# Kernel tuning notes

Measured on AMD Instinct MI355X. Metric: run time of the kernel, lower is better.

## Reference

```python
import jax, jax.numpy as jnp
import numpy as np

DIM = 1024
HEADS = 16
DK = DIM // HEADS
B, LQ, LKV = 2, 2048, 2048


def setup_inputs() -> dict:
    key = jax.random.key(0)
    ks = jax.random.split(key, 12)
    s = 1.0 / np.sqrt(DIM)
    return {
        "output": jax.random.normal(ks[0], (B, LQ, DIM), jnp.float32),
        "context": jax.random.normal(ks[1], (B, LKV, DIM), jnp.float32),
        # torch nn.Linear(dim, dim): store as [in, out] so y = x @ W + b
        "Wq": jax.random.normal(ks[2], (DIM, DIM), jnp.float32) * s,
        "bq": jax.random.normal(ks[3], (DIM,), jnp.float32) * s,
        "Wk": jax.random.normal(ks[4], (DIM, DIM), jnp.float32) * s,
        "bk": jax.random.normal(ks[5], (DIM,), jnp.float32) * s,
        "Wv": jax.random.normal(ks[6], (DIM, DIM), jnp.float32) * s,
        "bv": jax.random.normal(ks[7], (DIM,), jnp.float32) * s,
        # linear_out: in = 2*dim, out = dim
        "Wo": jax.random.normal(ks[8], (2 * DIM, DIM), jnp.float32) * (1.0 / np.sqrt(2 * DIM)),
        "bo": jax.random.normal(ks[9], (DIM,), jnp.float32) * (1.0 / np.sqrt(2 * DIM)),
    }


def _to_batches(x):
    # [B, L, dim] -> [B*H, L, dk], same layout as the torch reshape/permute
    b, l, _ = x.shape
    return x.reshape(b, l, HEADS, DK).transpose(0, 2, 1, 3).reshape(b * HEADS, l, DK)


def reference(output, context, Wq, bq, Wk, bk, Wv, bv, Wo, bo):
    b, lq, dim = output.shape
    q = _to_batches(output @ Wq + bq)     # [B*H, Lq, dk]
    k = _to_batches(context @ Wk + bk)    # [B*H, Lkv, dk]
    v = _to_batches(context @ Wv + bv)    # [B*H, Lkv, dk]

    scores = jnp.einsum('bqd,bkd->bqk', q, k) / jnp.sqrt(jnp.asarray(DK, q.dtype))
    attn = jax.nn.softmax(scores, axis=-1)            # [B*H, Lq, Lkv]; dropout = identity at eval
    ctx = jnp.einsum('bqk,bkd->bqd', attn, v)          # [B*H, Lq, dk]

    # Faithful to the original (non-standard) reshape:
    # scores.transpose(1,2).contiguous().view(B, -1, dim)
    concat = ctx.transpose(0, 2, 1).reshape(b, -1, dim)  # [B, Lq, dim] (permuted layout)
    combined = jnp.concatenate([concat, output], axis=2)  # [B, Lq, 2*dim]
    out = jnp.tanh(combined @ Wo + bo)                     # [B, Lq, dim]
    return (out, attn)
```

## Files before the change

### kernel.cpp

```cpp
#include <hip/hip_runtime.h>
#include <math.h>
#include <stdint.h>

#define DIM_ 1024
#define HEADS_ 16
#define DK_ 64
#define B_ 2
#define L_ 2048
#define BH_ (B_*HEADS_)
#define M_ (B_*L_)

typedef __attribute__((ext_vector_type(4))) float f32x4;
typedef __attribute__((ext_vector_type(8))) short bf16x8;
typedef __attribute__((ext_vector_type(4))) short bf16x4;

#define QSCALE 0.18033688f

static __device__ __forceinline__ short f2bf(float f) {
    uint32_t u = __builtin_bit_cast(uint32_t, f);
    u += 0x7fffu + ((u >> 16) & 1u);
    return (short)(u >> 16);
}
static __device__ __forceinline__ void gload16(const void* g, void* l) {
    __builtin_amdgcn_global_load_lds(
        (const __attribute__((address_space(1))) unsigned int*)g,
        (__attribute__((address_space(3))) unsigned int*)l, 16, 0, 0);
}

__global__ __launch_bounds__(256)
void prep(const float* __restrict__ xout, const float* __restrict__ xctx,
          const float* __restrict__ Wq, const float* __restrict__ Wk,
          const float* __restrict__ Wv, const float* __restrict__ Wo,
          short* __restrict__ xoutb, short* __restrict__ xctxb,
          short* __restrict__ WqT, short* __restrict__ WkT,
          short* __restrict__ WvT, short* __restrict__ WoT)
{
    __shared__ float ts[64][65];
    const int bid = blockIdx.x;
    const int tid = threadIdx.x;
    if (bid < 4096) {
        const int id = bid * 256 + tid;
        const int nA = (M_ * DIM_) / 8;
        const float* src = (id < nA) ? xout : xctx;
        short* dst = (id < nA) ? xoutb : xctxb;
        const int c = (id < nA) ? id : id - nA;
        const f32x4 v0 = *(const f32x4*)&src[(size_t)c * 8];
        const f32x4 v1 = *(const f32x4*)&src[(size_t)c * 8 + 4];
        bf16x8 o;
#pragma unroll
        for (int i = 0; i < 4; ++i) { o[i] = f2bf(v0[i]); o[4 + i] = f2bf(v1[i]); }
        *(bf16x8*)&dst[(size_t)c * 8] = o;
        return;
    }
    const int flat = bid - 4096;
    const int z = flat >> 9;
    const int rem = flat & 511;
    const int K = (z == 3) ? 2 * DIM_ : DIM_;
    const int k0 = (rem & 31) * 64;
    if (k0 >= K) return;
    const int n0 = (rem >> 5) * 64;
    const float* W = (z == 0) ? Wq : (z == 1) ? Wk : (z == 2) ? Wv : Wo;
    short* WT = (z == 0) ? WqT : (z == 1) ? WkT : (z == 2) ? WvT : WoT;
    {
        const int k = tid >> 2, noff = (tid & 3) * 16;
#pragma unroll
        for (int i = 0; i < 4; ++i)
            *(f32x4*)&ts[k][noff + i * 4] =
                *(const f32x4*)&W[(size_t)(k0 + k) * DIM_ + n0 + noff + i * 4];
    }
    __syncthreads();
    {
        const int n = tid >> 2, koff = (tid & 3) * 16;
#pragma unroll
        for (int c = 0; c < 2; ++c) {
            bf16x8 o;
#pragma unroll
            for (int i = 0; i < 8; ++i) o[i] = f2bf(ts[koff + c * 8 + i][n]);
            *(bf16x8*)&WT[(size_t)(n0 + n) * K + k0 + koff + c * 8] = o;
        }
    }
}

__global__ __launch_bounds__(256)
void qkv_mfma(const short* __restrict__ xoutb, const short* __restrict__ xctxb,
              const short* __restrict__ WqT, const short* __restrict__ WkT,
              const short* __restrict__ WvT,
              const float* __restrict__ bq, const float* __restrict__ bk,
              const float* __restrict__ bv,
              short* __restrict__ qh, short* __restrict__ kh, short* __restrict__ vT)
{
    const int z = blockIdx.z;
    const short* A  = (z == 0) ? xoutb : xctxb;
    const short* Bt = (z == 0) ? WqT : (z == 1) ? WkT : WvT;
    const float* bias = (z == 0) ? bq : (z == 1) ? bk : bv;

    const int flat = blockIdx.y * 8 + blockIdx.x;
    const int wgs = (flat & 7) * 32 + (flat >> 3);
    const int col0 = (wgs & 7) * 128;
    const int row0 = (wgs >> 3) * 128;
    const int tid = threadIdx.x;
    const int lane = tid & 63;
    const int w = tid >> 6;
    const int wm = (w >> 1) * 64, wn = (w & 1) * 64;
    const int l15 = lane & 15, g = lane >> 4;
    const int sub = lane >> 3, slt = lane & 7;

    __shared__ short As[128 * 64];
    __shared__ short Bs[128 * 64];

    const short* pA[4]; const short* pB[4]; short* ldsA[4]; short* ldsB[4];
#pragma unroll
    for (int i = 0; i < 4; ++i) {
        const int r = w * 32 + i * 8 + sub;
        const int sc = ((slt ^ (r & 7)) * 8);
        pA[i] = A  + (size_t)(row0 + r) * DIM_ + sc;
        pB[i] = Bt + (size_t)(col0 + r) * DIM_ + sc;
        ldsA[i] = &As[(w * 32 + i * 8) * 64];
        ldsB[i] = &Bs[(w * 32 + i * 8) * 64];
    }

    f32x4 acc[4][4];
#pragma unroll
    for (int mi = 0; mi < 4; ++mi)
#pragma unroll
        for (int ni = 0; ni < 4; ++ni) acc[mi][ni] = (f32x4)0.f;

    for (int k0 = 0; k0 < DIM_; k0 += 64) {
#pragma unroll
        for (int i = 0; i < 4; ++i) {
            gload16(pA[i] + k0, ldsA[i]);
            gload16(pB[i] + k0, ldsB[i]);
        }
        __syncthreads();
        bf16x8 af[4][2], bfr[4][2];
#pragma unroll
        for (int mi = 0; mi < 4; ++mi) {
            const int wa = wm + mi * 16 + l15;
#pragma unroll
            for (int ks = 0; ks < 2; ++ks)
                af[mi][ks] = *(const bf16x8*)&As[wa * 64 + (((ks * 4 + g) ^ (wa & 7)) * 8)];
        }
#pragma unroll
        for (int ni = 0; ni < 4; ++ni) {
            const int wb = wn + ni * 16 + l15;
#pragma unroll
            for (int ks = 0; ks < 2; ++ks)
                bfr[ni][ks] = *(const bf16x8*)&Bs[wb * 64 + (((ks * 4 + g) ^ (wb & 7)) * 8)];
        }
        __builtin_amdgcn_s_setprio(1);
#pragma unroll
        for (int mi = 0; mi < 4; ++mi)
#pragma unroll
            for (int ni = 0; ni < 4; ++ni)
#pragma unroll
                for (int ks = 0; ks < 2; ++ks)
                    acc[mi][ni] = __builtin_amdgcn_mfma_f32_16x16x32_bf16(af[mi][ks], bfr[ni][ks], acc[mi][ni], 0, 0, 0);
        __builtin_amdgcn_s_setprio(0);
        __syncthreads();
    }

#pragma unroll
    for (int ni = 0; ni < 4; ++ni) {
        const int col = col0 + wn + ni * 16 + l15;
        const int h = col >> 6, dk = col & 63;
        const float bb = bias[col];
#pragma unroll
        for (int mi = 0; mi < 4; ++mi) {
            const int rowb = row0 + wm + mi * 16 + g * 4;
            const int b = rowb >> 11;
            const int l = rowb & (L_ - 1);
            const int bh = b * 16 + h;
            if (z == 2) {
                bf16x4 o;
#pragma unroll
                for (int r = 0; r < 4; ++r) o[r] = f2bf(acc[mi][ni][r] + bb);
                *(bf16x4*)&vT[(size_t)(bh * 64 + dk) * L_ + l] = o;
            } else {
                short* dst = (z == 0) ? qh : kh;
                const float sc = (z == 0) ? QSCALE : 1.0f;
#pragma unroll
                for (int r = 0; r < 4; ++r)
                    dst[((size_t)bh * L_ + l + r) * DK_ + dk] = f2bf((acc[mi][ni][r] + bb) * sc);
            }
        }
    }
}

__global__ __launch_bounds__(512, 8)
void attn_mfma(const short* __restrict__ qh, const short* __restrict__ kh,
               const short* __restrict__ vT,
               float* __restrict__ attn, short* __restrict__ ctxTb)
{
    const int bid = blockIdx.x;
    const int wg = (bid & 7) * 128 + (bid >> 3);
    const int bh = wg >> 5;
    const int q0 = (wg & 31) * 64;

    const int tid = threadIdx.x;
    const int lane = tid & 63;
    const int w = tid >> 6;
    const int wq = w >> 1, wk = w & 1;
    const int l15 = lane & 15, g = lane >> 4;

    __shared__ short SM[17408];
    short* const Kb0 = SM;
    short* const Kb1 = SM + 4096;
    short* const Vb  = SM + 8192;
    short* const Psb = SM + 12288;
    float* const stat = (float*)(SM + 16896);

    const short* kbase = kh + (size_t)bh * (L_ * DK_);
    const short* vbase = vT + (size_t)bh * (DK_ * L_);

    const int lr = lane >> 3, ls = lane & 7;
    const int srow = w * 8 + lr;
    const short* kSrc = kbase + (size_t)srow * DK_ + ((ls ^ (srow & 7)) * 8);
    const short* vSrc = vbase + (size_t)srow * L_ + ((ls ^ (srow & 7)) * 8);

    bf16x8 qf[2];
#pragma unroll
    for (int ks = 0; ks < 2; ++ks)
        qf[ks] = *(const bf16x8*)&qh[((size_t)bh * L_ + q0 + wq * 16 + l15) * DK_ + ks * 32 + g * 8];

    int kbOff[2][2], vbOff[4];
#pragma unroll
    for (int cc = 0; cc < 2; ++cc)
#pragma unroll
        for (int ks = 0; ks < 2; ++ks) {
            const int row = wk * 32 + cc * 16 + l15;
            kbOff[cc][ks] = row * 64 + (((ks * 4 + g) ^ (row & 7)) * 8);
        }
#pragma unroll
    for (int nf = 0; nf < 4; ++nf) {
        const int row = nf * 16 + l15;
        vbOff[nf] = row * 64 + (((wk * 4 + g) ^ (row & 7)) * 8);
    }

    float m[4], s[4];
#pragma unroll
    for (int r = 0; r < 4; ++r) { m[r] = -1e30f; s[r] = 0.f; }

#pragma unroll
    for (int i = 0; i < 3; ++i)
        gload16(kSrc + (size_t)i * 64 * DK_, SM + (i << 12) + w * 512);
    asm volatile("s_waitcnt vmcnt(2)" ::: "memory");
    __builtin_amdgcn_sched_barrier(0);
    __builtin_amdgcn_s_barrier();

    for (int t = 0; t < 32; ++t) {
        if (t < 29)
            gload16(kSrc + (size_t)(t + 3) * 64 * DK_, SM + (((t + 3) & 3) << 12) + w * 512);
        const short* kb = SM + ((t & 3) << 12);
        f32x4 sa[2];
#pragma unroll
        for (int cc = 0; cc < 2; ++cc) sa[cc] = (f32x4)0.f;
        __builtin_amdgcn_s_setprio(1);
#pragma unroll
        for (int cc = 0; cc < 2; ++cc)
#pragma unroll
            for (int ks = 0; ks < 2; ++ks)
                sa[cc] = __builtin_amdgcn_mfma_f32_16x16x32_bf16(qf[ks], *(const bf16x8*)&kb[kbOff[cc][ks]], sa[cc], 0, 0, 0);
        __builtin_amdgcn_s_setprio(0);
#pragma unroll
        for (int r = 0; r < 4; ++r) {
            const float tm = fmaxf(sa[0][r], sa[1][r]);
            const float mn = fmaxf(m[r], tm);
            s[r] = s[r] * exp2f(m[r] - mn) + exp2f(sa[0][r] - mn) + exp2f(sa[1][r] - mn);
            m[r] = mn;
        }
        if (t < 29)       { asm volatile("s_waitcnt vmcnt(2)" ::: "memory"); }
        else if (t == 29) { asm volatile("s_waitcnt vmcnt(1)" ::: "memory"); }
        else if (t == 30) { asm volatile("s_waitcnt vmcnt(0)" ::: "memory"); }
        __builtin_amdgcn_sched_barrier(0);
        if (t < 31) __builtin_amdgcn_s_barrier();
    }
#pragma unroll
    for (int mask = 1; mask <= 8; mask <<= 1) {
#pragma unroll
        for (int r = 0; r < 4; ++r) {
            const float mo = __shfl_xor(m[r], mask);
            const float so = __shfl_xor(s[r], mask);
            const float mn = fmaxf(m[r], mo);
            s[r] = s[r] * exp2f(m[r] - mn) + so * exp2f(mo - mn);
            m[r] = mn;
        }
    }
    if (l15 == 0) {
#pragma unroll
        for (int r = 0; r < 4; ++r) {
            stat[((wq * 2 + wk) * 16 + g * 4 + r) * 2 + 0] = m[r];
            stat[((wq * 2 + wk) * 16 + g * 4 + r) * 2 + 1] = s[r];
        }
    }
    gload16(kSrc, SM + w * 512);
    asm volatile("s_waitcnt lgkmcnt(0)" ::: "memory");
    __builtin_amdgcn_s_barrier();
    float inv_s[4];
#pragma unroll
    for (int r = 0; r < 4; ++r) {
        const float m0 = stat[((wq * 2 + 0) * 16 + g * 4 + r) * 2 + 0];
        const float s0 = stat[((wq * 2 + 0) * 16 + g * 4 + r) * 2 + 1];
        const float m1 = stat[((wq * 2 + 1) * 16 + g * 4 + r) * 2 + 0];
        const float s1 = stat[((wq * 2 + 1) * 16 + g * 4 + r) * 2 + 1];
        const float mn = fmaxf(m0, m1);
        m[r] = mn;
        inv_s[r] = 1.0f / (s0 * exp2f(m0 - mn) + s1 * exp2f(m1 - mn));
    }

    f32x4 cacc[4];
#pragma unroll
    for (int nf = 0; nf < 4; ++nf) cacc[nf] = (f32x4)0.f;

    float* attnB = attn + ((size_t)bh * L_ + q0) * L_;

    asm volatile("s_waitcnt vmcnt(0)" ::: "memory");
    __builtin_amdgcn_sched_barrier(0);
    __builtin_amdgcn_s_barrier();

    for (int t = 0; t < 32; ++t) {
        if (t) {
            asm volatile("s_waitcnt vmcnt(8)" ::: "memory");
            __builtin_amdgcn_sched_barrier(0);
            __builtin_amdgcn_s_barrier();
        }
        gload16(vSrc + t * 64, Vb + w * 512);
        {
            const int tn = (t < 31) ? t + 1 : t;
            gload16(kSrc + (size_t)tn * 64 * DK_, ((t & 1) ? Kb0 : Kb1) + w * 512);
        }
        const short* kb = (t & 1) ? Kb1 : Kb0;
        f32x4 sa[2];
#pragma unroll
        for (int cc = 0; cc < 2; ++cc) sa[cc] = (f32x4)0.f;
        __builtin_amdgcn_s_setprio(1);
#pragma unroll
        for (int cc = 0; cc < 2; ++cc)
#pragma unroll
            for (int ks = 0; ks < 2; ++ks)
                sa[cc] = __builtin_amdgcn_mfma_f32_16x16x32_bf16(qf[ks], *(const bf16x8*)&kb[kbOff[cc][ks]], sa[cc], 0, 0, 0);
        __builtin_amdgcn_s_setprio(0);
#pragma unroll
        for (int cc = 0; cc < 2; ++cc)
#pragma unroll
            for (int r = 0; r < 4; ++r) {
                const float p = exp2f(sa[cc][r] - m[r]) * inv_s[r];
                Psb[(wq * 16 + g * 4 + r) * 72 + wk * 32 + cc * 16 + l15] = f2bf(p);
                __builtin_nontemporal_store(
                    p, attnB + (size_t)(wq * 16 + g * 4 + r) * L_ + t * 64 + wk * 32 + cc * 16 + l15);
            }
        asm volatile("s_waitcnt vmcnt(9) lgkmcnt(0)" ::: "memory");
        __builtin_amdgcn_sched_barrier(0);
        __builtin_amdgcn_s_barrier();
        const bf16x8 pa = *(const bf16x8*)&Psb[(wq * 16 + l15) * 72 + wk * 32 + g * 8];
        __builtin_amdgcn_s_setprio(1);
#pragma unroll
        for (int nf = 0; nf < 4; ++nf)
            cacc[nf] = __builtin_amdgcn_mfma_f32_16x16x32_bf16(pa, *(const bf16x8*)&Vb[vbOff[nf]], cacc[nf], 0, 0, 0);
        __builtin_amdgcn_s_setprio(0);
    }

    __syncthreads();
    float* scr = (float*)Kb0;
    float* scr1 = (float*)Kb1;
    if (wk) {
#pragma unroll
        for (int nf = 0; nf < 4; ++nf) {
            float* p = (nf < 2) ? scr : scr1;
            *(f32x4*)&p[(((wq * 2) + (nf & 1)) * 64 + lane) * 4] = cacc[nf];
        }
    }
    __syncthreads();
    if (!wk) {
#pragma unroll
        for (int nf = 0; nf < 4; ++nf) {
            const float* p = (nf < 2) ? scr : scr1;
            const f32x4 o = cacc[nf] + *(const f32x4*)&p[(((wq * 2) + (nf & 1)) * 64 + lane) * 4];
            bf16x4 ob;
#pragma unroll
            for (int r = 0; r < 4; ++r) ob[r] = f2bf(o[r]);
            *(bf16x4*)&ctxTb[(size_t)(bh * 64 + nf * 16 + l15) * L_ + q0 + wq * 16 + g * 4] = ob;
        }
    }
}

__global__ __launch_bounds__(256)
void out_mfma(const short* __restrict__ ctxTb, const short* __restrict__ xoutb,
              const short* __restrict__ WoT, const float* __restrict__ bo,
              float* __restrict__ out)
{
    const int flat = blockIdx.y * 16 + blockIdx.x;
    const int wgs = (flat & 7) * 64 + (flat >> 3);
    const int col0 = (wgs & 15) * 64;
    const int row0 = (wgs >> 4) * 128;
    const int tid = threadIdx.x;
    const int lane = tid & 63;
    const int w = tid >> 6;
    const int wm = (w >> 1) * 64, wn = (w & 1) * 32;
    const int l15 = lane & 15, g = lane >> 4;
    const int sub = lane >> 3, slt = lane & 7;

    __shared__ short As[128 * 64];
    __shared__ short Bs[64 * 64];

    const short* pA1[4]; const short* pA2[4]; const short* pB[2];
    short* ldsA[4]; short* ldsB[2];
#pragma unroll
    for (int i = 0; i < 4; ++i) {
        const int r = w * 32 + i * 8 + sub;
        const int rr = row0 + r;
        const int b = rr >> 11, l_ = rr & (L_ - 1);
        const int bh = b * 16 + (l_ >> 7), d = (l_ & 127) >> 1;
        const size_t off1 = ((size_t)(bh * 64 + d) << 11) + (size_t)((l_ & 1) << 10);
        const int sc = ((slt ^ (r & 7)) * 8);
        pA1[i] = ctxTb + off1 + sc;
        pA2[i] = xoutb + (size_t)rr * DIM_ + sc;
        ldsA[i] = &As[(w * 32 + i * 8) * 64];
    }
#pragma unroll
    for (int i = 0; i < 2; ++i) {
        const int r = w * 16 + i * 8 + sub;
        const int sc = ((slt ^ (r & 7)) * 8);
        pB[i]  = WoT + (size_t)(col0 + r) * (2 * DIM_) + sc;
        ldsB[i] = &Bs[(w * 16 + i * 8) * 64];
    }

    f32x4 acc[4][2];
#pragma unroll
    for (int mi = 0; mi < 4; ++mi)
#pragma unroll
        for (int ni = 0; ni < 2; ++ni) acc[mi][ni] = (f32x4)0.f;

    for (int k0 = 0; k0 < 2 * DIM_; k0 += 64) {
        const bool first = (k0 < DIM_);
        const int kk = first ? k0 : k0 - DIM_;
#pragma unroll
        for (int i = 0; i < 4; ++i)
            gload16(first ? (pA1[i] + kk) : (pA2[i] + kk), ldsA[i]);
#pragma unroll
        for (int i = 0; i < 2; ++i)
            gload16(pB[i] + k0, ldsB[i]);
        __syncthreads();
        bf16x8 af[4][2], bfr[2][2];
#pragma unroll
        for (int mi = 0; mi < 4; ++mi) {
            const int wa = wm + mi * 16 + l15;
#pragma unroll
            for (int ks = 0; ks < 2; ++ks)
                af[mi][ks] = *(const bf16x8*)&As[wa * 64 + (((ks * 4 + g) ^ (wa & 7)) * 8)];
        }
#pragma unroll
        for (int ni = 0; ni < 2; ++ni) {
            const int wb = wn + ni * 16 + l15;
#pragma unroll
            for (int ks = 0; ks < 2; ++ks)
                bfr[ni][ks] = *(const bf16x8*)&Bs[wb * 64 + (((ks * 4 + g) ^ (wb & 7)) * 8)];
        }
        __builtin_amdgcn_s_setprio(1);
#pragma unroll
        for (int mi = 0; mi < 4; ++mi)
#pragma unroll
            for (int ni = 0; ni < 2; ++ni)
#pragma unroll
                for (int ks = 0; ks < 2; ++ks)
                    acc[mi][ni] = __builtin_amdgcn_mfma_f32_16x16x32_bf16(af[mi][ks], bfr[ni][ks], acc[mi][ni], 0, 0, 0);
        __builtin_amdgcn_s_setprio(0);
        __syncthreads();
    }

#pragma unroll
    for (int ni = 0; ni < 2; ++ni) {
        const int col = col0 + wn + ni * 16 + l15;
        const float bb = bo[col];
#pragma unroll
        for (int mi = 0; mi < 4; ++mi) {
            const int rowb = row0 + wm + mi * 16 + g * 4;
#pragma unroll
            for (int r = 0; r < 4; ++r)
                out[(size_t)(rowb + r) * DIM_ + col] = tanhf(acc[mi][ni][r] + bb);
        }
    }
}

extern "C" void kernel_launch(void* const* d_in, const int* in_sizes, int n_in,
                              void* d_out, int out_size, void* d_ws, size_t ws_size,
                              hipStream_t stream)
{
    const float* xout = (const float*)d_in[0];
    const float* xctx = (const float*)d_in[1];
    const float* Wq = (const float*)d_in[2];
    const float* bq = (const float*)d_in[3];
    const float* Wk = (const float*)d_in[4];
    const float* bk = (const float*)d_in[5];
    const float* Wv = (const float*)d_in[6];
    const float* bv = (const float*)d_in[7];
    const float* Wo = (const float*)d_in[8];
    const float* bo = (const float*)d_in[9];

    float* out  = (float*)d_out;
    float* attn = out + (size_t)M_ * DIM_;

    short* ws = (short*)d_ws;
    short* xoutb = ws;
    short* xctxb = xoutb + (size_t)M_ * DIM_;
    short* WqT   = xctxb + (size_t)M_ * DIM_;
    short* WkT   = WqT + (size_t)DIM_ * DIM_;
    short* WvT   = WkT + (size_t)DIM_ * DIM_;
    short* WoT   = WvT + (size_t)DIM_ * DIM_;
    short* qh    = WoT + (size_t)2 * DIM_ * DIM_;
    short* kh    = qh + (size_t)BH_ * L_ * DK_;
    short* vT    = kh + (size_t)BH_ * L_ * DK_;
    short* ctxTb = vT + (size_t)BH_ * L_ * DK_;

    prep<<<6144, 256, 0, stream>>>(xout, xctx, Wq, Wk, Wv, Wo,
                                   xoutb, xctxb, WqT, WkT, WvT, WoT);
    qkv_mfma<<<dim3(8, 32, 3), 256, 0, stream>>>(
        xoutb, xctxb, WqT, WkT, WvT, bq, bk, bv, qh, kh, vT);
    attn_mfma<<<1024, 512, 0, stream>>>(qh, kh, vT, attn, ctxTb);
    out_mfma<<<dim3(16, 32), 256, 0, stream>>>(ctxTb, xoutb, WoT, bo, out);
}
```

Before: 279.2 us.

## Double-buffer LDS tiles in QKV projection and output GEMM kernels

Both the QKV projection GEMM and the output-projection GEMM now use two LDS buffers. The next K-tile's global-to-LDS load is issued before computing on the current tile, and each step ends with a single explicit waitcnt plus barrier. The aim is to hide global load latency behind MFMA work instead of stalling on every tile. In exchange the kernels use twice the shared memory, which may cut occupancy, and correctness now relies on manual vmcnt and barrier ordering.

```diff
diff --git a/kernel.cpp b/kernel.cpp
--- a/kernel.cpp
+++ b/kernel.cpp
@@ -105,18 +105,17 @@
     const int l15 = lane & 15, g = lane >> 4;
     const int sub = lane >> 3, slt = lane & 7;
 
-    __shared__ short As[128 * 64];
-    __shared__ short Bs[128 * 64];
-
-    const short* pA[4]; const short* pB[4]; short* ldsA[4]; short* ldsB[4];
+    __shared__ short As[2 * 128 * 64];
+    __shared__ short Bs[2 * 128 * 64];
+
+    const short* pA[4]; const short* pB[4]; int ldsOff[4];
 #pragma unroll
     for (int i = 0; i < 4; ++i) {
         const int r = w * 32 + i * 8 + sub;
         const int sc = ((slt ^ (r & 7)) * 8);
         pA[i] = A  + (size_t)(row0 + r) * DIM_ + sc;
         pB[i] = Bt + (size_t)(col0 + r) * DIM_ + sc;
-        ldsA[i] = &As[(w * 32 + i * 8) * 64];
-        ldsB[i] = &Bs[(w * 32 + i * 8) * 64];
+        ldsOff[i] = (w * 32 + i * 8) * 64;
     }
 
     f32x4 acc[4][4];
@@ -125,39 +124,68 @@
 #pragma unroll
         for (int ni = 0; ni < 4; ++ni) acc[mi][ni] = (f32x4)0.f;
 
-    for (int k0 = 0; k0 < DIM_; k0 += 64) {
-#pragma unroll
-        for (int i = 0; i < 4; ++i) {
-            gload16(pA[i] + k0, ldsA[i]);
-            gload16(pB[i] + k0, ldsB[i]);
-        }
-        __syncthreads();
-        bf16x8 af[4][2], bfr[4][2];
-#pragma unroll
-        for (int mi = 0; mi < 4; ++mi) {
-            const int wa = wm + mi * 16 + l15;
-#pragma unroll
-            for (int ks = 0; ks < 2; ++ks)
-                af[mi][ks] = *(const bf16x8*)&As[wa * 64 + (((ks * 4 + g) ^ (wa & 7)) * 8)];
-        }
-#pragma unroll
-        for (int ni = 0; ni < 4; ++ni) {
-            const int wb = wn + ni * 16 + l15;
-#pragma unroll
-            for (int ks = 0; ks < 2; ++ks)
-                bfr[ni][ks] = *(const bf16x8*)&Bs[wb * 64 + (((ks * 4 + g) ^ (wb & 7)) * 8)];
-        }
-        __builtin_amdgcn_s_setprio(1);
-#pragma unroll
-        for (int mi = 0; mi < 4; ++mi)
-#pragma unroll
-            for (int ni = 0; ni < 4; ++ni)
-#pragma unroll
-                for (int ks = 0; ks < 2; ++ks)
-                    acc[mi][ni] = __builtin_amdgcn_mfma_f32_16x16x32_bf16(af[mi][ks], bfr[ni][ks], acc[mi][ni], 0, 0, 0);
-        __builtin_amdgcn_s_setprio(0);
-        __syncthreads();
-    }
+#define QKV_STAGE(koff, buf)                                        \
+    {                                                               \
+        _Pragma("unroll")                                           \
+        for (int i = 0; i < 4; ++i) {                               \
+            gload16(pA[i] + (koff), As + (buf) * 8192 + ldsOff[i]); \
+            gload16(pB[i] + (koff), Bs + (buf) * 8192 + ldsOff[i]); \
+        }                                                           \
+    }
+
+#define QKV_COMPUTE(buf)                                                              \
+    {                                                                                 \
+        const short* as = As + (buf) * 8192;                                          \
+        const short* bs = Bs + (buf) * 8192;                                          \
+        bf16x8 af[4][2], bfr[4][2];                                                   \
+        _Pragma("unroll")                                                             \
+        for (int mi = 0; mi < 4; ++mi) {                                              \
+            const int wa = wm + mi * 16 + l15;                                        \
+            _Pragma("unroll")                                                         \
+            for (int ks = 0; ks < 2; ++ks)                                            \
+                af[mi][ks] = *(const bf16x8*)&as[wa * 64 + (((ks * 4 + g) ^ (wa & 7)) * 8)]; \
+        }                                                                             \
+        _Pragma("unroll")                                                             \
+        for (int ni = 0; ni < 4; ++ni) {                                              \
+            const int wb = wn + ni * 16 + l15;                                        \
+            _Pragma("unroll")                                                         \
+            for (int ks = 0; ks < 2; ++ks)                                            \
+                bfr[ni][ks] = *(const bf16x8*)&bs[wb * 64 + (((ks * 4 + g) ^ (wb & 7)) * 8)]; \
+        }                                                                             \
+        __builtin_amdgcn_s_setprio(1);                                                \
+        _Pragma("unroll")                                                             \
+        for (int mi = 0; mi < 4; ++mi)                                                \
+            _Pragma("unroll")                                                         \
+            for (int ni = 0; ni < 4; ++ni)                                            \
+                _Pragma("unroll")                                                     \
+                for (int ks = 0; ks < 2; ++ks)                                        \
+                    acc[mi][ni] = __builtin_amdgcn_mfma_f32_16x16x32_bf16(af[mi][ks], bfr[ni][ks], acc[mi][ni], 0, 0, 0); \
+        __builtin_amdgcn_s_setprio(0);                                                \
+    }
+
+    QKV_STAGE(0, 0);
+    asm volatile("s_waitcnt vmcnt(0)" ::: "memory");
+    __builtin_amdgcn_sched_barrier(0);
+    __builtin_amdgcn_s_barrier();
+
+    for (int kp = 0; kp < DIM_; kp += 128) {
+        QKV_STAGE(kp + 64, 1);
+        QKV_COMPUTE(0);
+        asm volatile("s_waitcnt vmcnt(0)" ::: "memory");
+        __builtin_amdgcn_sched_barrier(0);
+        __builtin_amdgcn_s_barrier();
+        if (kp + 128 < DIM_) {
+            QKV_STAGE(kp + 128, 0);
+            QKV_COMPUTE(1);
+            asm volatile("s_waitcnt vmcnt(0)" ::: "memory");
+            __builtin_amdgcn_sched_barrier(0);
+            __builtin_amdgcn_s_barrier();
+        } else {
+            QKV_COMPUTE(1);
+        }
+    }
+#undef QKV_STAGE
+#undef QKV_COMPUTE
 
 #pragma unroll
     for (int ni = 0; ni < 4; ++ni) {
@@ -399,11 +427,11 @@
     const int l15 = lane & 15, g = lane >> 4;
     const int sub = lane >> 3, slt = lane & 7;
 
-    __shared__ short As[128 * 64];
-    __shared__ short Bs[64 * 64];
+    __shared__ short As[2 * 128 * 64];
+    __shared__ short Bs[2 * 64 * 64];
 
     const short* pA1[4]; const short* pA2[4]; const short* pB[2];
-    short* ldsA[4]; short* ldsB[2];
+    int ldsAOff[4]; int ldsBOff[2];
 #pragma unroll
     for (int i = 0; i < 4; ++i) {
         const int r = w * 32 + i * 8 + sub;
@@ -414,14 +442,14 @@
         const int sc = ((slt ^ (r & 7)) * 8);
         pA1[i] = ctxTb + off1 + sc;
         pA2[i] = xoutb + (size_t)rr * DIM_ + sc;
-        ldsA[i] = &As[(w * 32 + i * 8) * 64];
+        ldsAOff[i] = (w * 32 + i * 8) * 64;
     }
 #pragma unroll
     for (int i = 0; i < 2; ++i) {
         const int r = w * 16 + i * 8 + sub;
         const int sc = ((slt ^ (r & 7)) * 8);
         pB[i]  = WoT + (size_t)(col0 + r) * (2 * DIM_) + sc;
-        ldsB[i] = &Bs[(w * 16 + i * 8) * 64];
+        ldsBOff[i] = (w * 16 + i * 8) * 64;
     }
 
     f32x4 acc[4][2];
@@ -430,42 +458,72 @@
 #pragma unroll
         for (int ni = 0; ni < 2; ++ni) acc[mi][ni] = (f32x4)0.f;
 
-    for (int k0 = 0; k0 < 2 * DIM_; k0 += 64) {
-        const bool first = (k0 < DIM_);
-        const int kk = first ? k0 : k0 - DIM_;
-#pragma unroll
-        for (int i = 0; i < 4; ++i)
-            gload16(first ? (pA1[i] + kk) : (pA2[i] + kk), ldsA[i]);
-#pragma unroll
-        for (int i = 0; i < 2; ++i)
-            gload16(pB[i] + k0, ldsB[i]);
-        __syncthreads();
-        bf16x8 af[4][2], bfr[2][2];
-#pragma unroll
-        for (int mi = 0; mi < 4; ++mi) {
-            const int wa = wm + mi * 16 + l15;
-#pragma unroll
-            for (int ks = 0; ks < 2; ++ks)
-                af[mi][ks] = *(const bf16x8*)&As[wa * 64 + (((ks * 4 + g) ^ (wa & 7)) * 8)];
-        }
-#pragma unroll
-        for (int ni = 0; ni < 2; ++ni) {
-            const int wb = wn + ni * 16 + l15;
-#pragma unroll
-            for (int ks = 0; ks < 2; ++ks)
-                bfr[ni][ks] = *(const bf16x8*)&Bs[wb * 64 + (((ks * 4 + g) ^ (wb & 7)) * 8)];
-        }
-        __builtin_amdgcn_s_setprio(1);
-#pragma unroll
-        for (int mi = 0; mi < 4; ++mi)
-#pragma unroll
-            for (int ni = 0; ni < 2; ++ni)
-#pragma unroll
-                for (int ks = 0; ks < 2; ++ks)
-                    acc[mi][ni] = __builtin_amdgcn_mfma_f32_16x16x32_bf16(af[mi][ks], bfr[ni][ks], acc[mi][ni], 0, 0, 0);
-        __builtin_amdgcn_s_setprio(0);
-        __syncthreads();
-    }
+#define OUT_STAGE(koff, buf)                                                     \
+    {                                                                            \
+        _Pragma("unroll")                                                        \
+        for (int i = 0; i < 4; ++i) {                                            \
+            const short* srcA = ((koff) < DIM_) ? (pA1[i] + (koff))              \
+                                                : (pA2[i] + ((koff) - DIM_));    \
+            gload16(srcA, As + (buf) * 8192 + ldsAOff[i]);                       \
+        }                                                                        \
+        _Pragma("unroll")                                                        \
+        for (int i = 0; i < 2; ++i)                                              \
+            gload16(pB[i] + (koff), Bs + (buf) * 4096 + ldsBOff[i]);             \
+    }
+
+#define OUT_COMPUTE(buf)                                                              \
+    {                                                                                 \
+        const short* as = As + (buf) * 8192;                                          \
+        const short* bs = Bs + (buf) * 4096;                                          \
+        bf16x8 af[4][2], bfr[2][2];                                                   \
+        _Pragma("unroll")                                                             \
+        for (int mi = 0; mi < 4; ++mi) {                                              \
+            const int wa = wm + mi * 16 + l15;                                        \
+            _Pragma("unroll")                                                         \
+            for (int ks = 0; ks < 2; ++ks)                                            \
+                af[mi][ks] = *(const bf16x8*)&as[wa * 64 + (((ks * 4 + g) ^ (wa & 7)) * 8)]; \
+        }                                                                             \
+        _Pragma("unroll")                                                             \
+        for (int ni = 0; ni < 2; ++ni) {                                              \
+            const int wb = wn + ni * 16 + l15;                                        \
+            _Pragma("unroll")                                                         \
+            for (int ks = 0; ks < 2; ++ks)                                            \
+                bfr[ni][ks] = *(const bf16x8*)&bs[wb * 64 + (((ks * 4 + g) ^ (wb & 7)) * 8)]; \
+        }                                                                             \
+        __builtin_amdgcn_s_setprio(1);                                                \
+        _Pragma("unroll")                                                             \
+        for (int mi = 0; mi < 4; ++mi)                                                \
+            _Pragma("unroll")                                                         \
+            for (int ni = 0; ni < 2; ++ni)                                            \
+                _Pragma("unroll")                                                     \
+                for (int ks = 0; ks < 2; ++ks)                                        \
+                    acc[mi][ni] = __builtin_amdgcn_mfma_f32_16x16x32_bf16(af[mi][ks], bfr[ni][ks], acc[mi][ni], 0, 0, 0); \
+        __builtin_amdgcn_s_setprio(0);                                                \
+    }
+
+    OUT_STAGE(0, 0);
+    asm volatile("s_waitcnt vmcnt(0)" ::: "memory");
+    __builtin_amdgcn_sched_barrier(0);
+    __builtin_amdgcn_s_barrier();
+
+    for (int kp = 0; kp < 2 * DIM_; kp += 128) {
+        OUT_STAGE(kp + 64, 1);
+        OUT_COMPUTE(0);
+        asm volatile("s_waitcnt vmcnt(0)" ::: "memory");
+        __builtin_amdgcn_sched_barrier(0);
+        __builtin_amdgcn_s_barrier();
+        if (kp + 128 < 2 * DIM_) {
+            OUT_STAGE(kp + 128, 0);
+            OUT_COMPUTE(1);
+            asm volatile("s_waitcnt vmcnt(0)" ::: "memory");
+            __builtin_amdgcn_sched_barrier(0);
+            __builtin_amdgcn_s_barrier();
+        } else {
+            OUT_COMPUTE(1);
+        }
+    }
+#undef OUT_STAGE
+#undef OUT_COMPUTE
 
 #pragma unroll
     for (int ni = 0; ni < 2; ++ni) {
```

New measurement: 282.0 us. No clear change (+1.0%).
